# Optimization experiments

Measured on AMD Instinct MI355X. Metric: run time of the kernel, lower is better.

The kernel has to match this reference:

```python
import jax, jax.numpy as jnp
import numpy as np

B, C, T, F, H = 4, 16, 1000, 96, 64
HID = C * F      # GRU hidden size = input_ch * input_freqs = 1536
IN = H * F       # GRU input size  = hidden_dim * input_freqs = 6144


def _conv(x, W, b):
    # Conv2d(in_ch, out_ch, kernel=(1,3), padding=(0,1)) -> same freq dim
    y = jax.lax.conv_general_dilated(
        x, W, window_strides=(1, 1), padding=((0, 0), (1, 1)),
        dimension_numbers=('NCHW', 'OIHW', 'NCHW'))
    return y + b[None, :, None, None]


def setup_inputs() -> dict:
    key = jax.random.key(0)
    ks = jax.random.split(key, 8)
    x = jax.random.normal(ks[0], (B, C, T, F), jnp.float32)
    h0 = jnp.zeros((B, HID), jnp.float32)
    sc_c = 1.0 / np.sqrt(C * 3)
    Wq = jax.random.normal(ks[1], (H, C, 1, 3), jnp.float32) * sc_c
    Wk = jax.random.normal(ks[2], (H, C, 1, 3), jnp.float32) * sc_c
    Wv = jax.random.normal(ks[3], (H, C, 1, 3), jnp.float32) * sc_c
    bq = jnp.zeros((H,), jnp.float32)
    bk = jnp.zeros((H,), jnp.float32)
    bv = jnp.zeros((H,), jnp.float32)
    sc_g = 1.0 / np.sqrt(HID)
    Wih = jax.random.normal(ks[4], (3 * HID, IN), jnp.float32) * sc_g
    Whh = jax.random.normal(ks[5], (3 * HID, HID), jnp.float32) * sc_g
    bih = jax.random.normal(ks[6], (3 * HID,), jnp.float32) * sc_g
    bhh = jax.random.normal(ks[7], (3 * HID,), jnp.float32) * sc_g
    return dict(x=x, h0=h0, Wq=Wq, bq=bq, Wk=Wk, bk=bk, Wv=Wv, bv=bv,
                Wih=Wih, Whh=Whh, bih=bih, bhh=bhh)


def reference(x, h0, Wq, bq, Wk, bk, Wv, bv, Wih, Whh, bih, bhh):
    b, c, t, f = x.shape
    h = Wq.shape[0]
    hid = h0.shape[-1]

    q = _conv(x, Wq, bq)   # [B,H,T,F]
    k = _conv(x, Wk, bk)
    v = _conv(x, Wv, bv)

    # per-timestep attention over freq axis: [B,T,F,F]
    w = jnp.einsum('bhtf,bhtg->btfg', q, k) / jnp.sqrt(jnp.float32(h))
    # joint 2D softmax over both freq axes (stable form, same math)
    w = w - jnp.max(w, axis=(2, 3), keepdims=True)
    w = jnp.exp(w)
    w = w / jnp.sum(w, axis=(2, 3), keepdims=True)

    a = jnp.einsum('btfg,bhtg->btfh', w, v)      # [B,T,F,H]
    seq = a.reshape(b, t, f * h)                 # flatten (F,H)

    # GRU (torch gate order r,z,n); precompute input projections
    gx = seq @ Wih.T + bih                       # [B,T,3*HID]

    def step(hc, gxt):
        gh = hc @ Whh.T + bhh
        r = jax.nn.sigmoid(gxt[:, :hid] + gh[:, :hid])
        z = jax.nn.sigmoid(gxt[:, hid:2 * hid] + gh[:, hid:2 * hid])
        n = jnp.tanh(gxt[:, 2 * hid:] + r * gh[:, 2 * hid:])
        hn = (1.0 - z) * n + z * hc
        return hn, hn

    hT, ys = jax.lax.scan(step, h0, gx.transpose(1, 0, 2))  # ys: [T,B,HID]
    o = ys.transpose(1, 0, 2).reshape(b, t, c, f).transpose(0, 2, 1, 3)  # [B,C,T,F]
    return o, hT
```

## Files before the change

kernel.cpp:

```cpp
#include <hip/hip_runtime.h>
#include <hip/hip_bf16.h>
#include <cstdint>
#include <cstddef>

typedef __bf16 bf16x8 __attribute__((ext_vector_type(8)));
typedef float  f32x4  __attribute__((ext_vector_type(4)));
typedef unsigned long long u64;

#define MFMA16(a, b, c) __builtin_amdgcn_mfma_f32_16x16x32_bf16((a), (b), (c), 0, 0, 0)

#define ASYNC_CP16(gsrc, ldst)                                                              \
    __builtin_amdgcn_global_load_lds((const __attribute__((address_space(1))) void*)(gsrc), \
                                     (__attribute__((address_space(3))) void*)(ldst), 16, 0, 0)

static constexpr int BN = 4, CN = 16, TN = 1000, FN = 96, HN = 64;
static constexpr int HID = 1536;
static constexpr int INQ = 6144;
static constexpr int G3  = 4608;

static constexpr size_t OFF_SEQ = 0;
static constexpr size_t OFF_WIH = 50331648;
static constexpr size_t OFF_GX  = OFF_WIH + 56623104;
static constexpr size_t OFF_H   = OFF_GX + 37748736;
static constexpr size_t OFF_BAR = OFF_H + 32768;

__device__ inline u64 pack4bf(float a, float b, float c, float d) {
    union { __bf16 h; unsigned short u; } x;
    u64 p;
    x.h = (__bf16)a; p = x.u;
    x.h = (__bf16)b; p |= (u64)x.u << 16;
    x.h = (__bf16)c; p |= (u64)x.u << 32;
    x.h = (__bf16)d; p |= (u64)x.u << 48;
    return p;
}

__global__ __launch_bounds__(256) void cvt_wih_kernel(const float* __restrict__ W,
                                                      __bf16* __restrict__ Wb) {
    size_t i0 = ((size_t)blockIdx.x * 256 + threadIdx.x) * 4;
    size_t stride = (size_t)gridDim.x * 256 * 4;
    for (size_t i = i0; i < (size_t)G3 * INQ; i += stride) {
        float4 v = *(const float4*)(W + i);
        Wb[i + 0] = (__bf16)v.x;
        Wb[i + 1] = (__bf16)v.y;
        Wb[i + 2] = (__bf16)v.z;
        Wb[i + 3] = (__bf16)v.w;
    }
}

__global__ __launch_bounds__(256) void conv_attn_kernel(
    const float* __restrict__ x,
    const float* __restrict__ Wq, const float* __restrict__ bq,
    const float* __restrict__ Wk, const float* __restrict__ bk,
    const float* __restrict__ Wv, const float* __restrict__ bv,
    __bf16* __restrict__ seqB) {
    const int bt  = blockIdx.x;
    const int tid = threadIdx.x;
    __bf16* srow = seqB + (size_t)bt * INQ;
    if (bt >= BN * TN) {
        for (int i = tid; i < INQ; i += 256) srow[i] = (__bf16)0.f;
        return;
    }
    const int b = bt / TN, t = bt % TN;

    __shared__ union __attribute__((aligned(16))) {
        struct {
            __bf16 xcolT[96][64];
            __bf16 wls[64][64];
        } c;
        __bf16 P[96][104];
    } u;
    __shared__ __attribute__((aligned(16))) __bf16 qT[96][72];
    __shared__ __attribute__((aligned(16))) __bf16 kT[96][72];
    __shared__ __attribute__((aligned(16))) __bf16 vhg[64][104];
    __shared__ float red[8];

    const int lane = tid & 63, wv = tid >> 6;
    const int wm = wv >> 1, wn = wv & 1;
    const int n16 = lane & 15, quad = lane >> 4;

    const float* xb = x + ((size_t)b * CN * TN + t) * FN;
    for (int idx = tid; idx < 96 * 64; idx += 256) {
        int f = idx >> 6, kk = idx & 63;
        float v = 0.f;
        if (kk < 48) {
            int c = kk / 3, d = kk % 3, fi = f + d - 1;
            if (fi >= 0 && fi < FN) v = xb[(size_t)c * TN * FN + fi];
        }
        u.c.xcolT[f][kk] = (__bf16)v;
    }

    auto load_w = [&](const float* W) {
        for (int idx = tid; idx < 64 * 64; idx += 256) {
            int h = idx >> 6, kk = idx & 63;
            u.c.wls[h][kk] = (__bf16)(kk < 48 ? W[h * 48 + kk] : 0.f);
        }
    };

    auto conv_T = [&](const float* bias, __bf16(*out)[72]) {
        f32x4 acc[3][2];
        for (int mt = 0; mt < 3; ++mt)
            for (int nt = 0; nt < 2; ++nt) acc[mt][nt] = f32x4{0.f, 0.f, 0.f, 0.f};
        #pragma unroll
        for (int ks = 0; ks < 2; ++ks) {
            bf16x8 a[3], bb[2];
            #pragma unroll
            for (int mt = 0; mt < 3; ++mt)
                a[mt] = *(const bf16x8*)&u.c.xcolT[(wm * 3 + mt) * 16 + n16][ks * 32 + quad * 8];
            #pragma unroll
            for (int nt = 0; nt < 2; ++nt)
                bb[nt] = *(const bf16x8*)&u.c.wls[(wn * 2 + nt) * 16 + n16][ks * 32 + quad * 8];
            #pragma unroll
            for (int mt = 0; mt < 3; ++mt)
                #pragma unroll
                for (int nt = 0; nt < 2; ++nt) acc[mt][nt] = MFMA16(a[mt], bb[nt], acc[mt][nt]);
        }
        #pragma unroll
        for (int mt = 0; mt < 3; ++mt)
            #pragma unroll
            for (int nt = 0; nt < 2; ++nt) {
                int h = (wn * 2 + nt) * 16 + n16;
                float bvv = bias[h];
                #pragma unroll
                for (int i = 0; i < 4; ++i) {
                    int f = (wm * 3 + mt) * 16 + quad * 4 + i;
                    out[f][h] = (__bf16)(acc[mt][nt][i] + bvv);
                }
            }
    };

    load_w(Wq);
    __syncthreads();
    conv_T(bq, qT);
    __syncthreads();
    load_w(Wk);
    __syncthreads();
    conv_T(bk, kT);
    __syncthreads();
    load_w(Wv);
    __syncthreads();
    {
        f32x4 acc[2][3];
        for (int mt = 0; mt < 2; ++mt)
            for (int nt = 0; nt < 3; ++nt) acc[mt][nt] = f32x4{0.f, 0.f, 0.f, 0.f};
        #pragma unroll
        for (int ks = 0; ks < 2; ++ks) {
            bf16x8 a[2], bb[3];
            #pragma unroll
            for (int mt = 0; mt < 2; ++mt)
                a[mt] = *(const bf16x8*)&u.c.wls[(wm * 2 + mt) * 16 + n16][ks * 32 + quad * 8];
            #pragma unroll
            for (int nt = 0; nt < 3; ++nt)
                bb[nt] = *(const bf16x8*)&u.c.xcolT[(wn * 3 + nt) * 16 + n16][ks * 32 + quad * 8];
            #pragma unroll
            for (int mt = 0; mt < 2; ++mt)
                #pragma unroll
                for (int nt = 0; nt < 3; ++nt) acc[mt][nt] = MFMA16(a[mt], bb[nt], acc[mt][nt]);
        }
        #pragma unroll
        for (int mt = 0; mt < 2; ++mt)
            #pragma unroll
            for (int nt = 0; nt < 3; ++nt) {
                int f = (wn * 3 + nt) * 16 + n16;
                #pragma unroll
                for (int i = 0; i < 4; ++i) {
                    int h = (wm * 2 + mt) * 16 + quad * 4 + i;
                    vhg[h][f] = (__bf16)(acc[mt][nt][i] + bv[h]);
                }
            }
    }
    __syncthreads();

    f32x4 sa[3][3];
    for (int mt = 0; mt < 3; ++mt)
        for (int nt = 0; nt < 3; ++nt) sa[mt][nt] = f32x4{0.f, 0.f, 0.f, 0.f};
    #pragma unroll
    for (int ks = 0; ks < 2; ++ks) {
        bf16x8 a[3], bb[3];
        #pragma unroll
        for (int mt = 0; mt < 3; ++mt)
            a[mt] = *(const bf16x8*)&qT[(wm * 3 + mt) * 16 + n16][ks * 32 + quad * 8];
        #pragma unroll
        for (int nt = 0; nt < 3; ++nt)
            bb[nt] = *(const bf16x8*)&kT[(wn * 3 + nt) * 16 + n16][ks * 32 + quad * 8];
        #pragma unroll
        for (int mt = 0; mt < 3; ++mt)
            #pragma unroll
            for (int nt = 0; nt < 3; ++nt) sa[mt][nt] = MFMA16(a[mt], bb[nt], sa[mt][nt]);
    }
    float mx = -1e30f;
    #pragma unroll
    for (int mt = 0; mt < 3; ++mt)
        #pragma unroll
        for (int nt = 0; nt < 3; ++nt)
            #pragma unroll
            for (int i = 0; i < 4; ++i) {
                float s = sa[mt][nt][i] * 0.125f;
                sa[mt][nt][i] = s;
                mx = fmaxf(mx, s);
            }
    #pragma unroll
    for (int m = 1; m < 64; m <<= 1) mx = fmaxf(mx, __shfl_xor(mx, m, 64));
    if (lane == 0) red[wv] = mx;
    __syncthreads();
    float M = fmaxf(fmaxf(red[0], red[1]), fmaxf(red[2], red[3]));
    float zs = 0.f;
    #pragma unroll
    for (int mt = 0; mt < 3; ++mt)
        #pragma unroll
        for (int nt = 0; nt < 3; ++nt) {
            int g = (wn * 3 + nt) * 16 + n16;
            #pragma unroll
            for (int i = 0; i < 4; ++i) {
                int f = (wm * 3 + mt) * 16 + quad * 4 + i;
                float e = __expf(sa[mt][nt][i] - M);
                zs += e;
                u.P[f][g] = (__bf16)e;
            }
        }
    #pragma unroll
    for (int m = 1; m < 64; m <<= 1) zs += __shfl_xor(zs, m, 64);
    if (lane == 0) red[4 + wv] = zs;
    __syncthreads();
    float zinv = 1.f / (red[4] + red[5] + red[6] + red[7]);

    f32x4 pa[3][2];
    for (int mt = 0; mt < 3; ++mt)
        for (int nt = 0; nt < 2; ++nt) pa[mt][nt] = f32x4{0.f, 0.f, 0.f, 0.f};
    #pragma unroll
    for (int ks = 0; ks < 3; ++ks) {
        bf16x8 a[3], bb[2];
        #pragma unroll
        for (int mt = 0; mt < 3; ++mt)
            a[mt] = *(const bf16x8*)&u.P[(wm * 3 + mt) * 16 + n16][ks * 32 + quad * 8];
        #pragma unroll
        for (int nt = 0; nt < 2; ++nt)
            bb[nt] = *(const bf16x8*)&vhg[(wn * 2 + nt) * 16 + n16][ks * 32 + quad * 8];
        #pragma unroll
        for (int mt = 0; mt < 3; ++mt)
            #pragma unroll
            for (int nt = 0; nt < 2; ++nt) pa[mt][nt] = MFMA16(a[mt], bb[nt], pa[mt][nt]);
    }
    #pragma unroll
    for (int mt = 0; mt < 3; ++mt)
        #pragma unroll
        for (int nt = 0; nt < 2; ++nt) {
            int h = (wn * 2 + nt) * 16 + n16;
            #pragma unroll
            for (int i = 0; i < 4; ++i) {
                int f = (wm * 3 + mt) * 16 + quad * 4 + i;
                srow[f * 64 + h] = (__bf16)(pa[mt][nt][i] * zinv);
            }
        }
}

__global__ __launch_bounds__(256) void gemm_kernel(const __bf16* __restrict__ A,
                                                   const __bf16* __restrict__ Bw,
                                                   const float* __restrict__ bih,
                                                   __bf16* __restrict__ gx) {
    const int bn = blockIdx.x;
    const int bm = blockIdx.y;
    const int tid = threadIdx.x;
    __shared__ __attribute__((aligned(16))) __bf16 As[128 * 64];
    __shared__ __attribute__((aligned(16))) __bf16 Bs[128 * 64];
    const int lane = tid & 63, wv = tid >> 6, wm = wv >> 1, wn = wv & 1;
    const int n16 = lane & 15, quad = lane >> 4;

    const int r  = tid >> 3;
    const int c8 = (tid & 7) * 8;
    const __bf16* ag = A  + ((size_t)(bm * 128 + r)) * INQ + c8;
    const __bf16* bg = Bw + ((size_t)(bn * 128 + r)) * INQ + c8;
    __bf16* as_dst = As + r * 64 + c8;
    __bf16* bs_dst = Bs + r * 64 + c8;

    f32x4 acc[4][4];
    for (int mt = 0; mt < 4; ++mt)
        for (int nt = 0; nt < 4; ++nt) acc[mt][nt] = f32x4{0.f, 0.f, 0.f, 0.f};

    for (int kt = 0; kt < 96; ++kt) {
        #pragma unroll
        for (int i = 0; i < 4; ++i) {
            ASYNC_CP16(ag + (size_t)i * 32 * INQ, as_dst + i * 32 * 64);
            ASYNC_CP16(bg + (size_t)i * 32 * INQ, bs_dst + i * 32 * 64);
        }
        ag += 64;
        bg += 64;
        __syncthreads();
        #pragma unroll
        for (int kk = 0; kk < 2; ++kk) {
            bf16x8 af[4], bf[4];
            #pragma unroll
            for (int mt = 0; mt < 4; ++mt)
                af[mt] = *(const bf16x8*)&As[(wm * 64 + mt * 16 + n16) * 64 + kk * 32 + quad * 8];
            #pragma unroll
            for (int nt = 0; nt < 4; ++nt)
                bf[nt] = *(const bf16x8*)&Bs[(wn * 64 + nt * 16 + n16) * 64 + kk * 32 + quad * 8];
            #pragma unroll
            for (int mt = 0; mt < 4; ++mt)
                #pragma unroll
                for (int nt = 0; nt < 4; ++nt) acc[mt][nt] = MFMA16(af[mt], bf[nt], acc[mt][nt]);
        }
        __syncthreads();
    }
    #pragma unroll
    for (int nt = 0; nt < 4; ++nt) {
        int n = bn * 128 + wn * 64 + nt * 16 + n16;
        float bvv = bih[n];
        #pragma unroll
        for (int mt = 0; mt < 4; ++mt) {
            int m0 = bm * 128 + wm * 64 + mt * 16 + quad * 4;
            #pragma unroll
            for (int i = 0; i < 4; ++i)
                gx[(size_t)(m0 + i) * G3 + n] = (__bf16)(acc[mt][nt][i] + bvv);
        }
    }
}

__global__ __launch_bounds__(256) void gru_kernel(const __bf16* __restrict__ gx,
                                                  const float* __restrict__ Whh,
                                                  const float* __restrict__ bhh,
                                                  const float* __restrict__ h0,
                                                  __bf16* __restrict__ hbuf,
                                                  unsigned* __restrict__ bar,
                                                  float* __restrict__ out) {
    const int blk = blockIdx.x;
    const int tid = threadIdx.x;
    const int u0 = blk * 4;
    constexpr int LDW = 1560;
    __shared__ __attribute__((aligned(16))) __bf16 Wl[12][LDW];
    __shared__ __attribute__((aligned(16))) __bf16 hl[4][LDW];
    __shared__ float part[4][4][16];
    __shared__ unsigned short hpack[4][4];

    unsigned* cnt    = bar + (blk & 15) * 32;
    unsigned* master = bar + 16 * 32;
    unsigned* genp   = bar + 17 * 32;

    auto bar_sync = [&](unsigned g) {
        __syncthreads();
        if (tid == 0) {
            unsigned old = __hip_atomic_fetch_add(cnt, 1u, __ATOMIC_RELAXED,
                                                  __HIP_MEMORY_SCOPE_AGENT);
            if (old + 1 == 24u * g) {
                unsigned mo = __hip_atomic_fetch_add(master, 1u, __ATOMIC_RELAXED,
                                                     __HIP_MEMORY_SCOPE_AGENT);
                if (mo + 1 == 16u * g)
                    __hip_atomic_store(genp, g, __ATOMIC_RELAXED, __HIP_MEMORY_SCOPE_AGENT);
            }
            while (__hip_atomic_load(genp, __ATOMIC_RELAXED, __HIP_MEMORY_SCOPE_AGENT) < g)
                __builtin_amdgcn_s_sleep(1);
        }
        __syncthreads();
    };

    for (int idx = tid; idx < 12 * HID; idx += 256) {
        int j = idx / HID, cc = idx % HID;
        int g = j >> 2, du = j & 3;
        Wl[j][cc] = (__bf16)Whh[(size_t)(g * HID + u0 + du) * HID + cc];
    }
    {
        u64* hb8 = (u64*)hbuf;
        for (int i = blk * 256 + tid; i < 1536; i += 384 * 256) {
            float4 v = *(const float4*)(h0 + i * 4);
            __hip_atomic_store(hb8 + i, pack4bf(v.x, v.y, v.z, v.w),
                               __ATOMIC_RELAXED, __HIP_MEMORY_SCOPE_AGENT);
        }
    }

    float hreg = 0.f;
    const int gb = tid >> 2, gu = tid & 3;
    float bhr = 0.f, bhz = 0.f, bhn = 0.f;
    if (tid < 16) {
        hreg = h0[gb * HID + u0 + gu];
        bhr = bhh[u0 + gu];
        bhz = bhh[HID + u0 + gu];
        bhn = bhh[2 * HID + u0 + gu];
    }

    bar_sync(1);

    const int lane = tid & 63, wvi = tid >> 6;
    const int n16 = lane & 15, quad = lane >> 4;
    const int kbase = wvi * 384;
    const int wr = (n16 < 12) ? n16 : 0;
    const int hr = n16 & 3;

    for (int t = 0; t < TN; ++t) {
        const u64* hs8 = (const u64*)(hbuf + (size_t)(t & 1) * INQ);
        #pragma unroll
        for (int j = tid; j < 1536; j += 256) {
            u64 v = __hip_atomic_load(hs8 + j, __ATOMIC_RELAXED, __HIP_MEMORY_SCOPE_AGENT);
            int bb = j / 384, cc = j % 384;
            *(u64*)&hl[bb][cc * 4] = v;
        }
        __syncthreads();

        f32x4 acc = f32x4{0.f, 0.f, 0.f, 0.f};
        #pragma unroll
        for (int ks = 0; ks < 12; ++ks) {
            int k = kbase + ks * 32 + quad * 8;
            bf16x8 av = *(const bf16x8*)&hl[hr][k];
            bf16x8 bv = *(const bf16x8*)&Wl[wr][k];
            acc = MFMA16(av, bv, acc);
        }
        if (quad == 0) {
            #pragma unroll
            for (int i = 0; i < 4; ++i) part[wvi][i][n16] = acc[i];
        }
        __syncthreads();

        if (tid < 16) {
            float gr = 0.f, gz = 0.f, gn = 0.f;
            #pragma unroll
            for (int w = 0; w < 4; ++w) {
                gr += part[w][gb][gu];
                gz += part[w][gb][4 + gu];
                gn += part[w][gb][8 + gu];
            }
            const __bf16* gxr = gx + (size_t)(gb * TN + t) * G3;
            float xr = (float)gxr[u0 + gu];
            float xz = (float)gxr[HID + u0 + gu];
            float xn = (float)gxr[2 * HID + u0 + gu];
            float rr = 1.f / (1.f + __expf(-(xr + gr + bhr)));
            float zz = 1.f / (1.f + __expf(-(xz + gz + bhz)));
            float nn = tanhf(xn + rr * (gn + bhn));
            float hn = (1.f - zz) * nn + zz * hreg;
            hreg = hn;
            union { __bf16 h; unsigned short us; } cv;
            cv.h = (__bf16)hn;
            hpack[gb][gu] = cv.us;
            int uu = u0 + gu;
            out[((size_t)(gb * CN + uu / FN) * TN + t) * FN + (uu % FN)] = hn;
            if (gu == 0) {
                u64 p = (u64)hpack[gb][0] | ((u64)hpack[gb][1] << 16) |
                        ((u64)hpack[gb][2] << 32) | ((u64)hpack[gb][3] << 48);
                u64* hd8 = (u64*)(hbuf + (size_t)((t + 1) & 1) * INQ);
                __hip_atomic_store(hd8 + gb * 384 + blk, p,
                                   __ATOMIC_RELAXED, __HIP_MEMORY_SCOPE_AGENT);
            }
        }
        bar_sync((unsigned)(t + 2));
    }
    if (tid < 16) out[(size_t)BN * CN * TN * FN + gb * HID + u0 + gu] = hreg;
}

extern "C" void kernel_launch(void* const* d_in, const int* in_sizes, int n_in,
                              void* d_out, int out_size, void* d_ws, size_t ws_size,
                              hipStream_t stream) {
    const float* x   = (const float*)d_in[0];
    const float* h0  = (const float*)d_in[1];
    const float* Wq  = (const float*)d_in[2];
    const float* bq  = (const float*)d_in[3];
    const float* Wk  = (const float*)d_in[4];
    const float* bk  = (const float*)d_in[5];
    const float* Wv  = (const float*)d_in[6];
    const float* bv  = (const float*)d_in[7];
    const float* Wih = (const float*)d_in[8];
    const float* Whh = (const float*)d_in[9];
    const float* bih = (const float*)d_in[10];
    const float* bhh = (const float*)d_in[11];
    float* out = (float*)d_out;
    char* ws = (char*)d_ws;
    __bf16* seqB = (__bf16*)(ws + OFF_SEQ);
    __bf16* WihB = (__bf16*)(ws + OFF_WIH);
    __bf16* gxB  = (__bf16*)(ws + OFF_GX);
    __bf16* hbuf = (__bf16*)(ws + OFF_H);
    unsigned* bar = (unsigned*)(ws + OFF_BAR);

    hipMemsetAsync((void*)bar, 0, 4096, stream);
    hipLaunchKernelGGL(cvt_wih_kernel, dim3(2048), dim3(256), 0, stream, Wih, WihB);
    hipLaunchKernelGGL(conv_attn_kernel, dim3(4096), dim3(256), 0, stream,
                       x, Wq, bq, Wk, bk, Wv, bv, seqB);
    hipLaunchKernelGGL(gemm_kernel, dim3(36, 32), dim3(256), 0, stream, seqB, WihB, bih, gxB);

    void* args[] = {(void*)&gxB, (void*)&Whh, (void*)&bhh, (void*)&h0,
                    (void*)&hbuf, (void*)&bar, (void*)&out};
    hipLaunchCooperativeKernel((void*)gru_kernel, dim3(384), dim3(256), args, 0, stream);
}
```

Measured before the change: 5.293 ms.

## Restructure GRU step: direct h loads, per-block gx layout with prefetch, distributed barrier flags

The input-projection GEMM now writes gx in a per-GRU-block layout, so each block's 12 gate values per timestep are contiguous. The recurrent loop prefetches the next step's gx before the grid barrier, which takes that load off the critical path. The h-state staging through LDS, and its extra __syncthreads, is replaced by atomic global loads straight into MFMA operands, with four independent accumulators to shorten the dependency chain. The barrier release now writes 16 separate generation flags so pollers do not all spin on one cache line. The cost is redundant global loads of h per wave and more release stores per step.

After: 8.626 ms. 1.63x slower.

```diff
diff --git a/kernel.cpp b/kernel.cpp
--- a/kernel.cpp
+++ b/kernel.cpp
@@ -256,7 +256,7 @@
 __global__ __launch_bounds__(256) void gemm_kernel(const __bf16* __restrict__ A,
                                                    const __bf16* __restrict__ Bw,
                                                    const float* __restrict__ bih,
-                                                   __bf16* __restrict__ gx) {
+                                                   __bf16* __restrict__ gxp) {
     const int bn = blockIdx.x;
     const int bm = blockIdx.y;
     const int tid = threadIdx.x;
@@ -305,17 +305,26 @@
     for (int nt = 0; nt < 4; ++nt) {
         int n = bn * 128 + wn * 64 + nt * 16 + n16;
         float bvv = bih[n];
+        int gate = n / HID;
+        int uu = n - gate * HID;
+        int ublk = uu >> 2, gu = uu & 3;
         #pragma unroll
         for (int mt = 0; mt < 4; ++mt) {
             int m0 = bm * 128 + wm * 64 + mt * 16 + quad * 4;
             #pragma unroll
-            for (int i = 0; i < 4; ++i)
-                gx[(size_t)(m0 + i) * G3 + n] = (__bf16)(acc[mt][nt][i] + bvv);
-        }
-    }
-}
-
-__global__ __launch_bounds__(256) void gru_kernel(const __bf16* __restrict__ gx,
+            for (int i = 0; i < 4; ++i) {
+                int m = m0 + i;
+                if (m < BN * TN) {
+                    int gb = m / TN, tt = m - gb * TN;
+                    gxp[((size_t)ublk * TN + tt) * 48 + gb * 12 + gate * 4 + gu] =
+                        (__bf16)(acc[mt][nt][i] + bvv);
+                }
+            }
+        }
+    }
+}
+
+__global__ __launch_bounds__(256) void gru_kernel(const __bf16* __restrict__ gxp,
                                                   const float* __restrict__ Whh,
                                                   const float* __restrict__ bhh,
                                                   const float* __restrict__ h0,
@@ -327,13 +336,12 @@
     const int u0 = blk * 4;
     constexpr int LDW = 1560;
     __shared__ __attribute__((aligned(16))) __bf16 Wl[12][LDW];
-    __shared__ __attribute__((aligned(16))) __bf16 hl[4][LDW];
     __shared__ float part[4][4][16];
     __shared__ unsigned short hpack[4][4];
 
     unsigned* cnt    = bar + (blk & 15) * 32;
     unsigned* master = bar + 16 * 32;
-    unsigned* genp   = bar + 17 * 32;
+    unsigned* mygen  = bar + (17 + (blk & 15)) * 32;
 
     auto bar_sync = [&](unsigned g) {
         __syncthreads();
@@ -343,10 +351,14 @@
             if (old + 1 == 24u * g) {
                 unsigned mo = __hip_atomic_fetch_add(master, 1u, __ATOMIC_RELAXED,
                                                      __HIP_MEMORY_SCOPE_AGENT);
-                if (mo + 1 == 16u * g)
-                    __hip_atomic_store(genp, g, __ATOMIC_RELAXED, __HIP_MEMORY_SCOPE_AGENT);
-            }
-            while (__hip_atomic_load(genp, __ATOMIC_RELAXED, __HIP_MEMORY_SCOPE_AGENT) < g)
+                if (mo + 1 == 16u * g) {
+                    #pragma unroll
+                    for (int i = 0; i < 16; ++i)
+                        __hip_atomic_store(bar + (17 + i) * 32, g, __ATOMIC_RELAXED,
+                                           __HIP_MEMORY_SCOPE_AGENT);
+                }
+            }
+            while (__hip_atomic_load(mygen, __ATOMIC_RELAXED, __HIP_MEMORY_SCOPE_AGENT) < g)
                 __builtin_amdgcn_s_sleep(1);
         }
         __syncthreads();
@@ -369,11 +381,16 @@
     float hreg = 0.f;
     const int gb = tid >> 2, gu = tid & 3;
     float bhr = 0.f, bhz = 0.f, bhn = 0.f;
+    float xr = 0.f, xz = 0.f, xn = 0.f;
+    const __bf16* gxme = gxp + (size_t)blk * TN * 48 + gb * 12 + gu;
     if (tid < 16) {
         hreg = h0[gb * HID + u0 + gu];
         bhr = bhh[u0 + gu];
         bhz = bhh[HID + u0 + gu];
         bhn = bhh[2 * HID + u0 + gu];
+        xr = (float)gxme[0];
+        xz = (float)gxme[4];
+        xn = (float)gxme[8];
     }
 
     bar_sync(1);
@@ -385,23 +402,22 @@
     const int hr = n16 & 3;
 
     for (int t = 0; t < TN; ++t) {
-        const u64* hs8 = (const u64*)(hbuf + (size_t)(t & 1) * INQ);
-        #pragma unroll
-        for (int j = tid; j < 1536; j += 256) {
-            u64 v = __hip_atomic_load(hs8 + j, __ATOMIC_RELAXED, __HIP_MEMORY_SCOPE_AGENT);
-            int bb = j / 384, cc = j % 384;
-            *(u64*)&hl[bb][cc * 4] = v;
-        }
-        __syncthreads();
-
-        f32x4 acc = f32x4{0.f, 0.f, 0.f, 0.f};
+        const u64* hfrag = (const u64*)(hbuf + (size_t)(t & 1) * INQ + hr * HID) +
+                           (kbase + quad * 8) / 4;
+        f32x4 a4[4];
+        #pragma unroll
+        for (int i = 0; i < 4; ++i) a4[i] = f32x4{0.f, 0.f, 0.f, 0.f};
         #pragma unroll
         for (int ks = 0; ks < 12; ++ks) {
-            int k = kbase + ks * 32 + quad * 8;
-            bf16x8 av = *(const bf16x8*)&hl[hr][k];
-            bf16x8 bv = *(const bf16x8*)&Wl[wr][k];
-            acc = MFMA16(av, bv, acc);
-        }
+            union { bf16x8 v; u64 q[2]; } ua;
+            ua.q[0] = __hip_atomic_load(hfrag + ks * 8, __ATOMIC_RELAXED,
+                                        __HIP_MEMORY_SCOPE_AGENT);
+            ua.q[1] = __hip_atomic_load(hfrag + ks * 8 + 1, __ATOMIC_RELAXED,
+                                        __HIP_MEMORY_SCOPE_AGENT);
+            bf16x8 bv = *(const bf16x8*)&Wl[wr][kbase + ks * 32 + quad * 8];
+            a4[ks & 3] = MFMA16(ua.v, bv, a4[ks & 3]);
+        }
+        f32x4 acc = (a4[0] + a4[1]) + (a4[2] + a4[3]);
         if (quad == 0) {
             #pragma unroll
             for (int i = 0; i < 4; ++i) part[wvi][i][n16] = acc[i];
@@ -416,10 +432,6 @@
                 gz += part[w][gb][4 + gu];
                 gn += part[w][gb][8 + gu];
             }
-            const __bf16* gxr = gx + (size_t)(gb * TN + t) * G3;
-            float xr = (float)gxr[u0 + gu];
-            float xz = (float)gxr[HID + u0 + gu];
-            float xn = (float)gxr[2 * HID + u0 + gu];
             float rr = 1.f / (1.f + __expf(-(xr + gr + bhr)));
             float zz = 1.f / (1.f + __expf(-(xz + gz + bhz)));
             float nn = tanhf(xn + rr * (gn + bhn));
@@ -437,6 +449,10 @@
                 __hip_atomic_store(hd8 + gb * 384 + blk, p,
                                    __ATOMIC_RELAXED, __HIP_MEMORY_SCOPE_AGENT);
             }
+            const __bf16* gnx = gxme + (size_t)(t + 1) * 48;
+            xr = (float)gnx[0];
+            xz = (float)gnx[4];
+            xn = (float)gnx[8];
         }
         bar_sync((unsigned)(t + 2));
     }
@@ -466,7 +482,7 @@
     __bf16* hbuf = (__bf16*)(ws + OFF_H);
     unsigned* bar = (unsigned*)(ws + OFF_BAR);
 
-    hipMemsetAsync((void*)bar, 0, 4096, stream);
+    hipMemsetAsync((void*)bar, 0, 8192, stream);
     hipLaunchKernelGGL(cvt_wih_kernel, dim3(2048), dim3(256), 0, stream, Wih, WihB);
     hipLaunchKernelGGL(conv_attn_kernel, dim3(4096), dim3(256), 0, stream,
                        x, Wq, bq, Wk, bk, Wv, bv, seqB);
```
